# Kernel optimization log

Measured on AMD Instinct MI355X. Metric: run time of the kernel, lower is better.

The kernel has to match this reference:

```python
import jax, jax.numpy as jnp
import numpy as np
from jax import lax

EPS = 1e-5

def setup_inputs() -> dict:
    key = jax.random.key(0)
    k1, k2, k3, k4, k5, k6 = jax.random.split(key, 6)
    x = jax.random.normal(k1, (1, 64, 31, 96, 96), dtype=jnp.float32)
    # small init scale keeps gate pre-activations in a sane range
    w = jax.random.normal(k2, (256, 64, 3, 3, 3), dtype=jnp.float32) * 0.05
    gamma = jax.random.uniform(k3, (256,), dtype=jnp.float32)
    beta = jax.random.normal(k4, (256,), dtype=jnp.float32) * 0.1
    mean = jax.random.normal(k5, (256,), dtype=jnp.float32) * 0.1
    var = jax.random.uniform(k6, (256,), dtype=jnp.float32) + 0.5
    return {"x": x, "w": w, "gamma": gamma, "beta": beta, "mean": mean, "var": var}

def _bcast(p):
    return p[None, :, None, None, None]

def reference(x, w, gamma, beta, mean, var):
    # Conv3d (bias=False), stride 1, padding 1, NCDHW
    gates = lax.conv_general_dilated(
        x, w, window_strides=(1, 1, 1), padding=[(1, 1)] * 3,
        dimension_numbers=("NCDHW", "OIDHW", "NCDHW"))
    # BatchNorm3d (inference, running stats)
    scale = gamma * lax.rsqrt(var + EPS)
    gates = gates * _bcast(scale) + _bcast(beta - mean * scale)
    C = 64  # out_channels
    Wx = jnp.tanh(gates[:, 0 * C:1 * C])
    ft = jax.nn.sigmoid(gates[:, 1 * C:2 * C])
    rt = jax.nn.sigmoid(gates[:, 2 * C:3 * C])
    X = jnp.tanh(gates[:, 3 * C:4 * C])  # act == 'tanh'
    # time axis (dim 2) to front: (D, B, C, H, W)
    Wt = jnp.moveaxis(Wx, 2, 0)
    Ft = jnp.moveaxis(ft, 2, 0)
    Rt = jnp.moveaxis(rt, 2, 0)
    Xt = jnp.moveaxis(X, 2, 0)
    # t = 0: Ct = 1 - ft (note: Wx unused at first step, per source)
    C0 = 1.0 - Ft[0]
    h0 = Rt[0] * C0 + (1.0 - Rt[0]) * Xt[0]
    def step(Ct, inp):
        wx, f, r, xx = inp
        Ct = f * Ct + (1.0 - f) * wx
        ht = r * Ct + (1.0 - r) * xx
        return Ct, ht
    _, hs = lax.scan(step, C0, (Wt[1:], Ft[1:], Rt[1:], Xt[1:]))
    hts = jnp.concatenate([h0[None], hs], axis=0)  # (D,B,C,H,W)
    return jnp.moveaxis(hts, 0, 2)  # (B,C,D,H,W)
```

## Files before the change

kernel.cpp:

```cpp
#include <hip/hip_runtime.h>
#include <cstddef>

#define CI_  64
#define CO_  256
#define DD_  31
#define HH_  96
#define WW_  96
#define HW_  (HH_*WW_)
#define DHW_ (DD_*HW_)
#define EPSV 1e-5f

#define PD_   33
#define PH_   98
#define PW_   98
#define PHW_  9604
#define PDHW_ 316932

#define S_COL 8
#define S_CIG 144
#define S_ROW 1152
#define S_DD  11520
#define NTASK 4320
#define NTASKP 4352
#define XH_N  (NTASKP*8)

#define NTILE 72
#define NBLK  (NTILE*DD_)

#define GBLK 32768
#define GDSTR ((size_t)NTILE * GBLK)

#define PREP_RB 216
#define PREP_PB 1239
#define PREP_TB 279
#define PREP_NB (PREP_RB + PREP_PB + PREP_TB)

typedef _Float16 half8   __attribute__((ext_vector_type(8)));
typedef _Float16 half4v  __attribute__((ext_vector_type(4)));
typedef float    float4v __attribute__((ext_vector_type(4)));

__device__ __forceinline__ void gl_lds16(const _Float16* g, _Float16* l) {
  __builtin_amdgcn_global_load_lds(
      (const __attribute__((address_space(1))) unsigned int*)(g),
      (__attribute__((address_space(3))) unsigned int*)(l), 16, 0, 0);
}

__global__ __launch_bounds__(256) void prep_k(const float* __restrict__ w,
                                              const float* __restrict__ x,
                                              _Float16* __restrict__ wr2,
                                              _Float16* __restrict__ xt) {
  const int bid = blockIdx.x;
  if (bid < PREP_RB) {
    int idx = bid * 256 + threadIdx.x;
    int lw   = idx & 15;
    int quad = (idx >> 4) & 3;
    int cog  = (idx >> 6) & 15;
    int tkc  = idx >> 10;
    int kc   = tkc & 1;
    int t    = tkc >> 1;
    int co   = cog * 16 + lw;
    int cib  = kc * 32 + quad * 8;
    half8 v;
#pragma unroll
    for (int s = 0; s < 8; s++)
      v[s] = (_Float16)w[(size_t)co * 1728 + (size_t)(cib + s) * 27 + t];
    *(half8*)(wr2 + (size_t)idx * 8) = v;
  } else if (bid < PREP_RB + PREP_PB) {
    int p = (bid - PREP_RB) * 256 + threadIdx.x;
    if (p >= PDHW_) return;
    int pd  = p / PHW_;
    int rem = p - pd * PHW_;
    int ph  = rem / PW_;
    int pw  = rem - ph * PW_;
    bool in = (pd >= 1) & (pd <= DD_) & (ph >= 1) & (ph <= HH_) & (pw >= 1) & (pw <= WW_);
    if (in) return;
    half8 z = (half8)(_Float16)0.f;
#pragma unroll
    for (int cig = 0; cig < 8; cig++)
      *(half8*)(xt + ((size_t)cig * PDHW_ + p) * 8) = z;
  } else {
    int idx = (bid - PREP_RB - PREP_PB) * 256 + threadIdx.x;
    if (idx >= 31 * 96 * 24) return;
    int wq  = idx % 24;
    int rem = idx / 24;
    int h   = rem % 96;
    int d   = rem / 96;
    const float* xp = x + (size_t)d * HW_ + (size_t)h * WW_ + wq * 4;
    size_t p0 = (size_t)(d + 1) * PHW_ + (size_t)(h + 1) * PW_ + (wq * 4 + 1);
#pragma unroll 1
    for (int cig = 0; cig < 8; cig++) {
      float4 vv[8];
#pragma unroll
      for (int s = 0; s < 8; s++)
        vv[s] = *(const float4*)(xp + (size_t)(cig * 8 + s) * DHW_);
#pragma unroll
      for (int k = 0; k < 4; k++) {
        half8 o;
#pragma unroll
        for (int s = 0; s < 8; s++) o[s] = (_Float16)(&vv[s].x)[k];
        *(half8*)(xt + ((size_t)cig * PDHW_ + p0 + k) * 8) = o;
      }
    }
  }
}

__device__ __forceinline__ float tanh_f(float v) {
  float t = __expf(-2.f * fabsf(v));
  return copysignf((1.f - t) * __builtin_amdgcn_rcpf(1.f + t), v);
}
__device__ __forceinline__ float sigm_f(float v) {
  return __builtin_amdgcn_rcpf(1.f + __expf(-v));
}

__global__ __launch_bounds__(512, 4) void conv_mfma_k(
    const _Float16* __restrict__ xt, const _Float16* __restrict__ wr2,
    const float* __restrict__ gamma, const float* __restrict__ beta,
    const float* __restrict__ mean, const float* __restrict__ var,
    _Float16* __restrict__ gates)
{
  __shared__ _Float16 xh[XH_N];

  const int bid  = blockIdx.x;
  const int flat = (bid & 7) * 279 + (bid >> 3);
  const int d    = flat / NTILE;
  const int bx   = flat - d * NTILE;
  const int wti  = bx % 6;
  const int hti  = bx / 6;
  const int h0   = hti * 8, w0 = wti * 16;

  const int tid  = threadIdx.x;
  const int lane = tid & 63;
  const int wave = __builtin_amdgcn_readfirstlane(tid >> 6);
  const int wm   = wave >> 2;
  const int wn   = wave & 3;
  const int lw   = lane & 15;
  const int quad = lane >> 4;

#pragma unroll 1
  for (int it = 0; it < 9; ++it) {
    const int wb = it * 512 + wave * 64;
    if (wb < NTASKP) {
      const int task = wb + lane;
      const int tt   = task < NTASK ? task : (NTASK - 1);
      int col = tt % 18;
      int rc  = tt / 18;
      int cig = rc & 7;
      int dr  = rc >> 3;
      int dd  = dr / 10;
      int row = dr - dd * 10;
      const _Float16* g = xt + (((size_t)cig * PDHW_ + (size_t)(d + dd) * PHW_ +
                                 (size_t)(h0 + row) * PW_ + (w0 + col)) << 3);
      gl_lds16(g, xh + (size_t)wb * 8);
    }
  }

  float4v acc[4][4];
#pragma unroll
  for (int m = 0; m < 4; m++)
#pragma unroll
    for (int j = 0; j < 4; j++) acc[m][j] = (float4v)0.f;

  __syncthreads();

  const int abase0 = quad * S_CIG + lw * S_COL + (wm * 4) * S_ROW;
  half8 af[6];
  half8 bf[4];
#pragma unroll
  for (int kd = 0; kd < 3; ++kd) {
#pragma unroll
    for (int kc = 0; kc < 2; ++kc) {
#pragma unroll
      for (int kw = 0; kw < 3; ++kw) {
        const int ab = abase0 + kd * S_DD + kc * (4 * S_CIG) + kw * S_COL;
#pragma unroll
        for (int r = 0; r < 6; ++r)
          af[r] = *(const half8*)(xh + ab + r * S_ROW);
#pragma unroll
        for (int kh = 0; kh < 3; ++kh) {
          const int t = (kd * 3 + kh) * 3 + kw;
          const _Float16* bp =
              wr2 + (((size_t)((t * 2 + kc) * 16 + wn * 4)) << 9) + (lane << 3);
#pragma unroll
          for (int j = 0; j < 4; ++j)
            bf[j] = *(const half8*)(bp + ((size_t)j << 9));
          __builtin_amdgcn_s_setprio(1);
#pragma unroll
          for (int j = 0; j < 4; ++j) {
            acc[0][j] = __builtin_amdgcn_mfma_f32_16x16x32_f16(af[kh    ], bf[j], acc[0][j], 0, 0, 0);
            acc[1][j] = __builtin_amdgcn_mfma_f32_16x16x32_f16(af[kh + 1], bf[j], acc[1][j], 0, 0, 0);
            acc[2][j] = __builtin_amdgcn_mfma_f32_16x16x32_f16(af[kh + 2], bf[j], acc[2][j], 0, 0, 0);
            acc[3][j] = __builtin_amdgcn_mfma_f32_16x16x32_f16(af[kh + 3], bf[j], acc[3][j], 0, 0, 0);
          }
          __builtin_amdgcn_s_setprio(0);
        }
      }
    }
  }

  __syncthreads();

  const bool istanh = (wn == 0) || (wn == 3);
#pragma unroll
  for (int j = 0; j < 4; j++) {
    const int co = wn * 64 + j * 16 + lw;
    const int c  = j * 16 + lw;
    const float s  = gamma[co] * rsqrtf(var[co] + EPSV);
    const float bb = fmaf(-mean[co], s, beta[co]);
    const int cbase = c << 10;
    const int key   = (c & 7) << 4;
#pragma unroll
    for (int m = 0; m < 4; m++) {
#pragma unroll
      for (int reg = 0; reg < 4; reg++) {
        float v = fmaf(acc[m][j][reg], s, bb);
        _Float16 a = (_Float16)(istanh ? tanh_f(v) : sigm_f(v));
        const int sp = wm * 64 + m * 16 + quad * 4 + reg;
        *(_Float16*)((char*)xh + cbase + (((sp << 3) + (wn << 1)) ^ key)) = a;
      }
    }
  }
  __syncthreads();

  _Float16* gb = gates + (size_t)(d * NTILE + bx) * GBLK;
#pragma unroll
  for (int r = 0; r < 8; r++) {
    const int c = wave * 8 + r;
    const half8 rv = *(const half8*)((const char*)xh + (c << 10) +
                                     ((lane ^ (c & 7)) << 4));
    *(half8*)(gb + (size_t)c * 512 + lane * 8) = rv;
  }
}

__global__ __launch_bounds__(256) void recurrence_k(const _Float16* __restrict__ gates,
                                                    float* __restrict__ out) {
  const int idx = blockIdx.x * 256 + threadIdx.x;
  const int sp  = idx & 127;
  const int t2  = idx >> 7;
  const int c   = t2 / NTILE;
  const int bx  = t2 - c * NTILE;
  const int hti = bx / 6, wti = bx - hti * 6;
  const int h   = hti * 8 + (sp >> 4);
  const int w   = wti * 16 + (sp & 15);

  const _Float16* g0 = gates + (size_t)bx * GBLK + (size_t)c * 512 + sp * 4;
  float* op = out + (size_t)c * DHW_ + (size_t)h * WW_ + w;

#define LD(dv) (*(const half4v*)(g0 + (size_t)(dv) * GDSTR))
  half4v p[4];
#pragma unroll
  for (int i = 0; i < 4; i++) p[i] = LD(i);

  float C = 0.f;
#pragma unroll
  for (int d = 0; d < DD_; d++) {
    half4v cur = p[d & 3];
    if (d + 4 < DD_) p[d & 3] = LD(d + 4);
    float wx = (float)cur[0], f = (float)cur[1];
    float r  = (float)cur[2], x = (float)cur[3];
    C = (d == 0) ? (1.f - f) : fmaf(f, C - wx, wx);
    op[(size_t)d * HW_] = fmaf(r, C - x, x);
  }
#undef LD
}

extern "C" void kernel_launch(void* const* d_in, const int* in_sizes, int n_in,
                              void* d_out, int out_size, void* d_ws, size_t ws_size,
                              hipStream_t stream) {
  const float* x     = (const float*)d_in[0];
  const float* w     = (const float*)d_in[1];
  const float* gamma = (const float*)d_in[2];
  const float* beta  = (const float*)d_in[3];
  const float* mean  = (const float*)d_in[4];
  const float* var   = (const float*)d_in[5];
  float* out = (float*)d_out;

  _Float16* wr2   = (_Float16*)d_ws;
  _Float16* xt    = (_Float16*)((char*)d_ws + 884736);
  _Float16* gates = (_Float16*)((char*)d_ws + 884736 + 40567296);

  prep_k<<<PREP_NB, 256, 0, stream>>>(w, x, wr2, xt);
  conv_mfma_k<<<NBLK, 512, 0, stream>>>(xt, wr2, gamma, beta, mean, var, gates);
  recurrence_k<<<(64 * NTILE * 128) / 256, 256, 0, stream>>>(gates, out);
}
```

Baseline: 406.8 us.

## Switch conv MFMA from 16x16x32 to 32x32x16 with new weight layout

Replaces the 4x4 grid of 16x16x32 MFMA tiles per wave with a 2x2 grid of 32x32x16 MFMA tiles, and reorders the prepacked weight layout to match the new B-operand fragment shape. The A fragments are now loaded per k-quarter directly from LDS instead of reusing a sliding window of six rows across kh, and the s_setprio hints are dropped. The goal is fewer MFMA issues and fewer B-fragment loads per FLOP, at the cost of losing A-operand reuse across kh and a different epilogue index mapping.

```diff
diff --git a/kernel.cpp b/kernel.cpp
--- a/kernel.cpp
+++ b/kernel.cpp
@@ -38,6 +38,7 @@
 typedef _Float16 half8   __attribute__((ext_vector_type(8)));
 typedef _Float16 half4v  __attribute__((ext_vector_type(4)));
 typedef float    float4v __attribute__((ext_vector_type(4)));
+typedef float    float16v __attribute__((ext_vector_type(16)));
 
 __device__ __forceinline__ void gl_lds16(const _Float16* g, _Float16* l) {
   __builtin_amdgcn_global_load_lds(
@@ -47,24 +48,22 @@
 
 __global__ __launch_bounds__(256) void prep_k(const float* __restrict__ w,
                                               const float* __restrict__ x,
-                                              _Float16* __restrict__ wr2,
+                                              _Float16* __restrict__ wr3,
                                               _Float16* __restrict__ xt) {
   const int bid = blockIdx.x;
   if (bid < PREP_RB) {
     int idx = bid * 256 + threadIdx.x;
-    int lw   = idx & 15;
-    int quad = (idx >> 4) & 3;
-    int cog  = (idx >> 6) & 15;
-    int tkc  = idx >> 10;
-    int kc   = tkc & 1;
-    int t    = tkc >> 1;
-    int co   = cog * 16 + lw;
-    int cib  = kc * 32 + quad * 8;
+    int lane = idx & 63;
+    int cob  = (idx >> 6) & 7;
+    int kq   = (idx >> 9) & 3;
+    int t    = idx >> 11;
+    int co   = cob * 32 + (lane & 31);
+    int cib  = kq * 16 + (lane >> 5) * 8;
     half8 v;
 #pragma unroll
     for (int s = 0; s < 8; s++)
       v[s] = (_Float16)w[(size_t)co * 1728 + (size_t)(cib + s) * 27 + t];
-    *(half8*)(wr2 + (size_t)idx * 8) = v;
+    *(half8*)(wr3 + (size_t)idx * 8) = v;
   } else if (bid < PREP_RB + PREP_PB) {
     int p = (bid - PREP_RB) * 256 + threadIdx.x;
     if (p >= PDHW_) return;
@@ -113,7 +112,7 @@
 }
 
 __global__ __launch_bounds__(512, 4) void conv_mfma_k(
-    const _Float16* __restrict__ xt, const _Float16* __restrict__ wr2,
+    const _Float16* __restrict__ xt, const _Float16* __restrict__ wr3,
     const float* __restrict__ gamma, const float* __restrict__ beta,
     const float* __restrict__ mean, const float* __restrict__ var,
     _Float16* __restrict__ gates)
@@ -133,8 +132,6 @@
   const int wave = __builtin_amdgcn_readfirstlane(tid >> 6);
   const int wm   = wave >> 2;
   const int wn   = wave & 3;
-  const int lw   = lane & 15;
-  const int quad = lane >> 4;
 
 #pragma unroll 1
   for (int it = 0; it < 9; ++it) {
@@ -154,44 +151,38 @@
     }
   }
 
-  float4v acc[4][4];
-#pragma unroll
-  for (int m = 0; m < 4; m++)
-#pragma unroll
-    for (int j = 0; j < 4; j++) acc[m][j] = (float4v)0.f;
+  float16v acc[2][2];
+#pragma unroll
+  for (int a = 0; a < 2; a++)
+#pragma unroll
+    for (int b = 0; b < 2; b++)
+#pragma unroll
+      for (int r = 0; r < 16; r++) acc[a][b][r] = 0.f;
 
   __syncthreads();
 
-  const int abase0 = quad * S_CIG + lw * S_COL + (wm * 4) * S_ROW;
-  half8 af[6];
-  half8 bf[4];
+  const int abase0 = (wm * 4 + ((lane >> 4) & 1)) * S_ROW +
+                     (lane >> 5) * S_CIG + (lane & 15) * S_COL;
 #pragma unroll
   for (int kd = 0; kd < 3; ++kd) {
 #pragma unroll
-    for (int kc = 0; kc < 2; ++kc) {
+    for (int kh = 0; kh < 3; ++kh) {
 #pragma unroll
       for (int kw = 0; kw < 3; ++kw) {
-        const int ab = abase0 + kd * S_DD + kc * (4 * S_CIG) + kw * S_COL;
-#pragma unroll
-        for (int r = 0; r < 6; ++r)
-          af[r] = *(const half8*)(xh + ab + r * S_ROW);
-#pragma unroll
-        for (int kh = 0; kh < 3; ++kh) {
-          const int t = (kd * 3 + kh) * 3 + kw;
+        const int t  = (kd * 3 + kh) * 3 + kw;
+        const int ab = abase0 + kd * S_DD + kh * S_ROW + kw * S_COL;
+#pragma unroll
+        for (int kq = 0; kq < 4; ++kq) {
+          half8 a0 = *(const half8*)(xh + ab + kq * 2 * S_CIG);
+          half8 a1 = *(const half8*)(xh + ab + kq * 2 * S_CIG + 2 * S_ROW);
           const _Float16* bp =
-              wr2 + (((size_t)((t * 2 + kc) * 16 + wn * 4)) << 9) + (lane << 3);
-#pragma unroll
-          for (int j = 0; j < 4; ++j)
-            bf[j] = *(const half8*)(bp + ((size_t)j << 9));
-          __builtin_amdgcn_s_setprio(1);
-#pragma unroll
-          for (int j = 0; j < 4; ++j) {
-            acc[0][j] = __builtin_amdgcn_mfma_f32_16x16x32_f16(af[kh    ], bf[j], acc[0][j], 0, 0, 0);
-            acc[1][j] = __builtin_amdgcn_mfma_f32_16x16x32_f16(af[kh + 1], bf[j], acc[1][j], 0, 0, 0);
-            acc[2][j] = __builtin_amdgcn_mfma_f32_16x16x32_f16(af[kh + 2], bf[j], acc[2][j], 0, 0, 0);
-            acc[3][j] = __builtin_amdgcn_mfma_f32_16x16x32_f16(af[kh + 3], bf[j], acc[3][j], 0, 0, 0);
-          }
-          __builtin_amdgcn_s_setprio(0);
+              wr3 + (((size_t)((t * 4 + kq) * 8 + wn * 2)) << 9) + (lane << 3);
+          half8 b0 = *(const half8*)(bp);
+          half8 b1 = *(const half8*)(bp + 512);
+          acc[0][0] = __builtin_amdgcn_mfma_f32_32x32x16_f16(a0, b0, acc[0][0], 0, 0, 0);
+          acc[0][1] = __builtin_amdgcn_mfma_f32_32x32x16_f16(a0, b1, acc[0][1], 0, 0, 0);
+          acc[1][0] = __builtin_amdgcn_mfma_f32_32x32x16_f16(a1, b0, acc[1][0], 0, 0, 0);
+          acc[1][1] = __builtin_amdgcn_mfma_f32_32x32x16_f16(a1, b1, acc[1][1], 0, 0, 0);
         }
       }
     }
@@ -201,20 +192,21 @@
 
   const bool istanh = (wn == 0) || (wn == 3);
 #pragma unroll
-  for (int j = 0; j < 4; j++) {
-    const int co = wn * 64 + j * 16 + lw;
-    const int c  = j * 16 + lw;
+  for (int nb = 0; nb < 2; ++nb) {
+    const int cl = nb * 32 + (lane & 31);
+    const int co = wn * 64 + cl;
     const float s  = gamma[co] * rsqrtf(var[co] + EPSV);
     const float bb = fmaf(-mean[co], s, beta[co]);
-    const int cbase = c << 10;
-    const int key   = (c & 7) << 4;
-#pragma unroll
-    for (int m = 0; m < 4; m++) {
-#pragma unroll
-      for (int reg = 0; reg < 4; reg++) {
-        float v = fmaf(acc[m][j][reg], s, bb);
+    const int cbase = cl << 10;
+    const int key   = (cl & 7) << 4;
+#pragma unroll
+    for (int mb = 0; mb < 2; ++mb) {
+#pragma unroll
+      for (int reg = 0; reg < 16; ++reg) {
+        const int r  = (reg & 3) + 8 * (reg >> 2) + 4 * (lane >> 5);
+        const int sp = (wm * 4 + mb * 2 + (r >> 4)) * 16 + (r & 15);
+        float v = fmaf(acc[mb][nb][reg], s, bb);
         _Float16 a = (_Float16)(istanh ? tanh_f(v) : sigm_f(v));
-        const int sp = wm * 64 + m * 16 + quad * 4 + reg;
         *(_Float16*)((char*)xh + cbase + (((sp << 3) + (wn << 1)) ^ key)) = a;
       }
     }
@@ -274,11 +266,11 @@
   const float* var   = (const float*)d_in[5];
   float* out = (float*)d_out;
 
-  _Float16* wr2   = (_Float16*)d_ws;
+  _Float16* wr3   = (_Float16*)d_ws;
   _Float16* xt    = (_Float16*)((char*)d_ws + 884736);
   _Float16* gates = (_Float16*)((char*)d_ws + 884736 + 40567296);
 
-  prep_k<<<PREP_NB, 256, 0, stream>>>(w, x, wr2, xt);
-  conv_mfma_k<<<NBLK, 512, 0, stream>>>(xt, wr2, gamma, beta, mean, var, gates);
+  prep_k<<<PREP_NB, 256, 0, stream>>>(w, x, wr3, xt);
+  conv_mfma_k<<<NBLK, 512, 0, stream>>>(xt, wr3, gamma, beta, mean, var, gates);
   recurrence_k<<<(64 * NTILE * 128) / 256, 256, 0, stream>>>(gates, out);
 }
```

Result: slower. 486.3 us (+19.5%).
